# Optimization experiments

Measured on AMD Instinct MI355X. Metric: run time of the kernel, lower is better.

## Reference

```python
import jax, jax.numpy as jnp
import numpy as np

N_NODES = 50000
N_EDGES = 800000
IN_F = 512
H_F = 32
HEADS = 8
N_CLS = 40
NEG_SLOPE = 0.2


def gat_conv(h, W, al, ar, b, src, dst, n_heads, d_out):
    """DGL-style GATConv. h: [N, F_in]; W: [F_in, n_heads*d_out];
    al, ar: [n_heads, d_out]; b: [n_heads*d_out]. Returns [N, n_heads, d_out]."""
    n = h.shape[0]
    feat = (h @ W).reshape(n, n_heads, d_out)            # [N, H, D]
    el = jnp.sum(feat * al[None], axis=-1)               # [N, H]
    er = jnp.sum(feat * ar[None], axis=-1)               # [N, H]
    e = jax.nn.leaky_relu(el[src] + er[dst], NEG_SLOPE)  # [E, H]
    # numerically stable edge softmax per destination node
    m = jax.ops.segment_max(e, dst, num_segments=n)      # [N, H]
    m = jnp.where(jnp.isfinite(m), m, 0.0)
    ee = jnp.exp(e - m[dst])                             # [E, H]
    den = jax.ops.segment_sum(ee, dst, num_segments=n)   # [N, H]
    alpha = ee / jnp.maximum(den[dst], 1e-9)             # [E, H]
    msg = alpha[:, :, None] * feat[src]                  # [E, H, D]
    rst = jax.ops.segment_sum(msg, dst, num_segments=n)  # [N, H, D]
    return rst + b.reshape(1, n_heads, d_out)


def setup_inputs() -> dict:
    key = jax.random.key(0)
    ks = jax.random.split(key, 16)
    hid = H_F * HEADS
    s = lambda fan: 1.0 / np.sqrt(fan)
    return {
        "in_feat": jax.random.normal(ks[0], (N_NODES, IN_F), jnp.float32),
        "src": jax.random.randint(ks[1], (N_EDGES,), 0, N_NODES, jnp.int32),
        "dst": jax.random.randint(ks[2], (N_EDGES,), 0, N_NODES, jnp.int32),
        "W0": jax.random.normal(ks[3], (IN_F, hid), jnp.float32) * s(IN_F),
        "al0": jax.random.normal(ks[4], (HEADS, H_F), jnp.float32) * s(H_F),
        "ar0": jax.random.normal(ks[5], (HEADS, H_F), jnp.float32) * s(H_F),
        "b0": jnp.zeros((hid,), jnp.float32),
        "W1": jax.random.normal(ks[6], (hid, hid), jnp.float32) * s(hid),
        "al1": jax.random.normal(ks[7], (HEADS, H_F), jnp.float32) * s(H_F),
        "ar1": jax.random.normal(ks[8], (HEADS, H_F), jnp.float32) * s(H_F),
        "b1": jnp.zeros((hid,), jnp.float32),
        "W2": jax.random.normal(ks[9], (hid, N_CLS), jnp.float32) * s(hid),
        "al2": jax.random.normal(ks[10], (1, N_CLS), jnp.float32) * s(N_CLS),
        "ar2": jax.random.normal(ks[11], (1, N_CLS), jnp.float32) * s(N_CLS),
        "b2": jnp.zeros((N_CLS,), jnp.float32),
    }


def reference(in_feat, src, dst, W0, al0, ar0, b0, W1, al1, ar1, b1,
              W2, al2, ar2, b2):
    n = in_feat.shape[0]
    # layer 0 + ReLU (dropout p=0.0 is identity) + flatten heads
    h = gat_conv(in_feat, W0, al0, ar0, b0, src, dst, HEADS, H_F)
    h = jax.nn.relu(h).reshape(n, -1)
    # layer 1
    h = gat_conv(h, W1, al1, ar1, b1, src, dst, HEADS, H_F)
    h = jax.nn.relu(h).reshape(n, -1)
    # output layer, single head, no activation
    h = gat_conv(h, W2, al2, ar2, b2, src, dst, 1, N_CLS)
    return h.reshape(n, -1)
```

## Files before the change

kernel.cpp:

```cpp
#include <hip/hip_runtime.h>
#include <hip/hip_bf16.h>

#define N_NODES 50000
#define N_EDGES 800000
#define IN_F 512
#define HID 256
#define HEADS 8
#define DHEAD 32
#define N_CLS 40
#define NCLS_PAD 64

typedef __bf16 bf16x8 __attribute__((ext_vector_type(8)));
typedef float f32x4 __attribute__((ext_vector_type(4)));

#define AT_AL0 0
#define AT_AR0 256
#define AT_AL1 512
#define AT_AR1 768
#define AT_AL2 1024
#define AT_AR2 1088
#define AT_B0  1152
#define AT_B1  1408
#define AT_B2  1664
#define AT_SZ  1792

__device__ __forceinline__ float ldflag(const void* p, long long i, int isbf) {
  return isbf ? __bfloat162float(((const __hip_bfloat16*)p)[i])
              : ((const float*)p)[i];
}
__device__ __forceinline__ float blo(unsigned u) { return __uint_as_float(u << 16); }
__device__ __forceinline__ float bhi(unsigned u) { return __uint_as_float(u & 0xffff0000u); }
__device__ __forceinline__ unsigned pk2(float a, float b) {
  unsigned x = __bfloat16_as_ushort(__float2bfloat16(a));
  unsigned y = __bfloat16_as_ushort(__float2bfloat16(b));
  return x | (y << 16);
}

__global__ void k_detect_prep(const unsigned short* __restrict__ raw, int* __restrict__ flag,
                              const void* al0, const void* ar0, const void* al1, const void* ar1,
                              const void* al2, const void* ar2, const void* b0, const void* b1,
                              const void* b2, float* __restrict__ att, int* __restrict__ cursor) {
  __shared__ int cnt[256];
  int t = threadIdx.x;
  for (int i = t; i < N_NODES; i += 256) cursor[i] = 0;
  int c = 0;
  for (int i = t; i < 8192; i += 256) {
    int e = (raw[i] >> 7) & 0xFF;
    if (e >= 0x90) c++;
  }
  cnt[t] = c;
  __syncthreads();
  for (int s = 128; s; s >>= 1) {
    if (t < s) cnt[t] += cnt[t + s];
    __syncthreads();
  }
  __shared__ int sflag;
  if (t == 0) { sflag = (cnt[0] > 64) ? 0 : 1; *flag = sflag; }
  __syncthreads();
  int isbf = sflag;
  att[AT_AL0 + t] = ldflag(al0, t, isbf);
  att[AT_AR0 + t] = ldflag(ar0, t, isbf);
  att[AT_AL1 + t] = ldflag(al1, t, isbf);
  att[AT_AR1 + t] = ldflag(ar1, t, isbf);
  att[AT_B0 + t]  = ldflag(b0, t, isbf);
  att[AT_B1 + t]  = ldflag(b1, t, isbf);
  if (t < N_CLS) {
    att[AT_AL2 + t] = ldflag(al2, t, isbf);
    att[AT_AR2 + t] = ldflag(ar2, t, isbf);
    att[AT_B2 + t]  = ldflag(b2, t, isbf);
  }
}

__global__ void k_hist(const int* __restrict__ dst, int* __restrict__ cnt) {
  int e = blockIdx.x * blockDim.x + threadIdx.x;
  if (e < N_EDGES) atomicAdd(&cnt[dst[e]], 1);
}

#define SCAN_B 512
#define SCAN_NB ((N_NODES + SCAN_B - 1) / SCAN_B)

__global__ __launch_bounds__(SCAN_B) void k_scan_blocks(const int* __restrict__ deg,
                                                        int* __restrict__ excl,
                                                        int* __restrict__ partial) {
  __shared__ int buf[SCAN_B];
  int t = threadIdx.x;
  int i = blockIdx.x * SCAN_B + t;
  int v = (i < N_NODES) ? deg[i] : 0;
  buf[t] = v;
  __syncthreads();
  for (int off = 1; off < SCAN_B; off <<= 1) {
    int x = (t >= off) ? buf[t - off] : 0;
    __syncthreads();
    buf[t] += x;
    __syncthreads();
  }
  if (i < N_NODES) excl[i] = buf[t] - v;
  if (t == SCAN_B - 1) partial[blockIdx.x] = buf[t];
}

__global__ void k_scan_partials(int* __restrict__ partial, int* __restrict__ rowptr) {
  __shared__ int buf[SCAN_NB];
  int t = threadIdx.x;
  if (t < SCAN_NB) buf[t] = partial[t];
  __syncthreads();
  if (t == 0) {
    int run = 0;
    for (int b = 0; b < SCAN_NB; b++) { int v = buf[b]; buf[b] = run; run += v; }
    rowptr[N_NODES] = run;
  }
  __syncthreads();
  if (t < SCAN_NB) partial[t] = buf[t];
}

__global__ void k_scan_add(int* __restrict__ rowptr, const int* __restrict__ partial,
                           int* __restrict__ cursor) {
  int i = blockIdx.x * blockDim.x + threadIdx.x;
  if (i < N_NODES) {
    rowptr[i] += partial[i / SCAN_B];
    cursor[i] = 0;
  }
}

__global__ void k_scatter(const int* __restrict__ src, const int* __restrict__ dst,
                          const int* __restrict__ rowptr, int* __restrict__ cursor,
                          int* __restrict__ csr_src) {
  int e = blockIdx.x * blockDim.x + threadIdx.x;
  if (e < N_EDGES) {
    int d = dst[e];
    int pos = rowptr[d] + atomicAdd(&cursor[d], 1);
    csr_src[pos] = src[e];
  }
}

#define TW0 (HID * IN_F)
#define TW1 (TW0 + HID * HID)
#define TW2 (TW1 + NCLS_PAD * HID)
__global__ void k_transpose_all(const void* __restrict__ W0, const void* __restrict__ W1,
                                const void* __restrict__ W2,
                                __hip_bfloat16* __restrict__ w0t, __hip_bfloat16* __restrict__ w1t,
                                __hip_bfloat16* __restrict__ w2t, const int* __restrict__ flag) {
  int isbf = *flag;
  int i = blockIdx.x * blockDim.x + threadIdx.x;
  if (i < TW0) {
    int n = i >> 9, k = i & 511;
    w0t[i] = __float2bfloat16(ldflag(W0, (long long)k * HID + n, isbf));
  } else if (i < TW1) {
    int j = i - TW0;
    int n = j >> 8, k = j & 255;
    w1t[j] = __float2bfloat16(ldflag(W1, (long long)k * HID + n, isbf));
  } else if (i < TW2) {
    int j = i - TW1;
    int n = j >> 8, k = j & 255;
    float v = (n < N_CLS) ? ldflag(W2, (long long)k * N_CLS + n, isbf) : 0.f;
    w2t[j] = __float2bfloat16(v);
  }
}

__device__ __forceinline__ uint4 loadA(const void* A, int isbf, int ga, int M, int K, int off) {
  uint4 av = make_uint4(0u, 0u, 0u, 0u);
  if (ga < M) {
    if (isbf) {
      av = *(const uint4*)((const __hip_bfloat16*)A + (size_t)ga * K + off);
    } else {
      const float* ap = (const float*)A + (size_t)ga * K + off;
      float4 f1 = *(const float4*)ap;
      float4 f2 = *(const float4*)(ap + 4);
      av.x = pk2(f1.x, f1.y); av.y = pk2(f1.z, f1.w);
      av.z = pk2(f2.x, f2.y); av.w = pk2(f2.z, f2.w);
    }
  }
  return av;
}

__global__ __launch_bounds__(256) void k_gemm64(const void* __restrict__ A,
                                                const __hip_bfloat16* __restrict__ Bt,
                                                __hip_bfloat16* __restrict__ C,
                                                int M, int K, int N,
                                                const int* __restrict__ flag, int force_bf,
                                                const float* __restrict__ al,
                                                const float* __restrict__ ar,
                                                float* __restrict__ el,
                                                float* __restrict__ er, int fuse_eler) {
  __shared__ unsigned short As[64][40];
  __shared__ unsigned short Bs[64][40];
  const int isbf = force_bf ? 1 : *flag;
  int nblk = N >> 6;
  int per = nblk << 3;
  int g = blockIdx.x / per;
  int i2 = blockIdx.x - g * per;
  int mb = g * 8 + (i2 & 7);
  int nb = i2 >> 3;
  int m0 = mb * 64, n0 = nb * 64;
  if (m0 >= M) return;
  int tid = threadIdx.x;
  int lrow = tid >> 2;
  int lcol = (tid & 3) * 8;
  int wave = tid >> 6, lane = tid & 63;
  int wm = (wave >> 1) * 32, wn = (wave & 1) * 32;
  int lm = lane & 15, quad = lane >> 4;
  f32x4 acc[2][2] = {};
  uint4 av = loadA(A, isbf, m0 + lrow, M, K, lcol);
  uint4 bv = *(const uint4*)(Bt + (size_t)(n0 + lrow) * K + lcol);
  for (int k0 = 0; k0 < K; k0 += 32) {
    __syncthreads();
    *(uint4*)(&As[lrow][lcol]) = av;
    *(uint4*)(&Bs[lrow][lcol]) = bv;
    __syncthreads();
    uint4 avn = make_uint4(0u, 0u, 0u, 0u), bvn = make_uint4(0u, 0u, 0u, 0u);
    if (k0 + 32 < K) {
      avn = loadA(A, isbf, m0 + lrow, M, K, k0 + 32 + lcol);
      bvn = *(const uint4*)(Bt + (size_t)(n0 + lrow) * K + k0 + 32 + lcol);
    }
    bf16x8 af[2], bfr[2];
    #pragma unroll
    for (int i = 0; i < 2; i++) {
      af[i]  = *(const bf16x8*)(&As[wm + i * 16 + lm][quad * 8]);
      bfr[i] = *(const bf16x8*)(&Bs[wn + i * 16 + lm][quad * 8]);
    }
    #pragma unroll
    for (int mi = 0; mi < 2; mi++)
      #pragma unroll
      for (int ni = 0; ni < 2; ni++)
        acc[mi][ni] = __builtin_amdgcn_mfma_f32_16x16x32_bf16(af[mi], bfr[ni], acc[mi][ni], 0, 0, 0);
    av = avn; bv = bvn;
  }
  #pragma unroll
  for (int mi = 0; mi < 2; mi++)
    #pragma unroll
    for (int ni = 0; ni < 2; ni++)
      #pragma unroll
      for (int r = 0; r < 4; r++) {
        int gm = m0 + wm + mi * 16 + quad * 4 + r;
        int gn = n0 + wn + ni * 16 + lm;
        if (gm < M) C[(size_t)gm * N + gn] = __float2bfloat16(acc[mi][ni][r]);
      }
  if (fuse_eler) {
    int hg = (n0 + wn) >> 5;
    float ala[2], ara[2];
    #pragma unroll
    for (int ni = 0; ni < 2; ni++) {
      ala[ni] = al[hg * DHEAD + ni * 16 + lm];
      ara[ni] = ar[hg * DHEAD + ni * 16 + lm];
    }
    #pragma unroll
    for (int mi = 0; mi < 2; mi++)
      #pragma unroll
      for (int r = 0; r < 4; r++) {
        float pl = acc[mi][0][r] * ala[0] + acc[mi][1][r] * ala[1];
        float pr = acc[mi][0][r] * ara[0] + acc[mi][1][r] * ara[1];
        #pragma unroll
        for (int d = 1; d < 16; d <<= 1) {
          pl += __shfl_xor(pl, d, 16);
          pr += __shfl_xor(pr, d, 16);
        }
        int gm = m0 + wm + mi * 16 + quad * 4 + r;
        if (lm == 0 && gm < M) {
          el[gm * HEADS + hg] = pl;
          er[gm * HEADS + hg] = pr;
        }
      }
  }
}

__global__ void k_eler2(const __hip_bfloat16* __restrict__ feat2,
                        const float* __restrict__ al, const float* __restrict__ ar,
                        float* __restrict__ el, float* __restrict__ er) {
  int n = blockIdx.x * blockDim.x + threadIdx.x;
  if (n >= N_NODES) return;
  const __hip_bfloat16* f = feat2 + (size_t)n * NCLS_PAD;
  float sl = 0.f, sr = 0.f;
  for (int d = 0; d < N_CLS; d++) {
    float v = __bfloat162float(f[d]);
    sl += v * al[d];
    sr += v * ar[d];
  }
  el[n] = sl;
  er[n] = sr;
}

__global__ __launch_bounds__(256) void k_aggregate8(const int* __restrict__ rowptr,
                                                    const int* __restrict__ csr_src,
                                                    const uint4* __restrict__ feat_rows,
                                                    const float* __restrict__ el,
                                                    const float* __restrict__ er,
                                                    const float* __restrict__ bias,
                                                    __hip_bfloat16* __restrict__ out) {
  __shared__ float lds_acc[8][256];
  __shared__ float lds_l[8][32];
  int n = blockIdx.x;
  int t = threadIdx.x;
  int slot = t >> 5;
  int c = t & 31;
  int hh = c >> 2;
  float er_n = er[n * HEADS + hh];
  int beg = rowptr[n], end = rowptr[n + 1];
  float l = 0.f;
  float acc[8] = {0.f, 0.f, 0.f, 0.f, 0.f, 0.f, 0.f, 0.f};
  int i = beg + slot;
  for (; i + 8 < end; i += 16) {
    int s1 = csr_src[i];
    int s2 = csr_src[i + 8];
    float el1 = el[s1 * HEADS + hh];
    float el2 = el[s2 * HEADS + hh];
    uint4 f1 = feat_rows[(size_t)s1 * 32 + c];
    uint4 f2 = feat_rows[(size_t)s2 * 32 + c];
    float x1 = el1 + er_n, x2 = el2 + er_n;
    float e1 = x1 > 0.f ? x1 : 0.2f * x1;
    float e2 = x2 > 0.f ? x2 : 0.2f * x2;
    float p1 = __expf(fminf(e1, 60.f));
    float p2 = __expf(fminf(e2, 60.f));
    l += p1 + p2;
    acc[0] += p1 * blo(f1.x) + p2 * blo(f2.x); acc[1] += p1 * bhi(f1.x) + p2 * bhi(f2.x);
    acc[2] += p1 * blo(f1.y) + p2 * blo(f2.y); acc[3] += p1 * bhi(f1.y) + p2 * bhi(f2.y);
    acc[4] += p1 * blo(f1.z) + p2 * blo(f2.z); acc[5] += p1 * bhi(f1.z) + p2 * bhi(f2.z);
    acc[6] += p1 * blo(f1.w) + p2 * blo(f2.w); acc[7] += p1 * bhi(f1.w) + p2 * bhi(f2.w);
  }
  if (i < end) {
    int s = csr_src[i];
    float elv = el[s * HEADS + hh];
    uint4 fv = feat_rows[(size_t)s * 32 + c];
    float x = elv + er_n;
    float e = x > 0.f ? x : 0.2f * x;
    float p = __expf(fminf(e, 60.f));
    l += p;
    acc[0] += p * blo(fv.x); acc[1] += p * bhi(fv.x);
    acc[2] += p * blo(fv.y); acc[3] += p * bhi(fv.y);
    acc[4] += p * blo(fv.z); acc[5] += p * bhi(fv.z);
    acc[6] += p * blo(fv.w); acc[7] += p * bhi(fv.w);
  }
  *(float4*)&lds_acc[slot][c * 8]     = make_float4(acc[0], acc[1], acc[2], acc[3]);
  *(float4*)&lds_acc[slot][c * 8 + 4] = make_float4(acc[4], acc[5], acc[6], acc[7]);
  lds_l[slot][c] = l;
  __syncthreads();
  float a = 0.f, L = 0.f;
  #pragma unroll
  for (int s2 = 0; s2 < 8; s2++) { a += lds_acc[s2][t]; L += lds_l[s2][t >> 3]; }
  float o = a / fmaxf(L, 1e-9f) + bias[t];
  o = fmaxf(o, 0.f);
  out[(size_t)n * HID + t] = __float2bfloat16(o);
}

__global__ __launch_bounds__(256) void k_aggregate1(const int* __restrict__ rowptr,
                                                    const int* __restrict__ csr_src,
                                                    const uint4* __restrict__ fr2,
                                                    const float* __restrict__ el,
                                                    const float* __restrict__ er,
                                                    const float* __restrict__ bias,
                                                    void* __restrict__ out,
                                                    const int* __restrict__ flag) {
  __shared__ float lds_acc[32][64];
  __shared__ float lds_l[32][8];
  int isbf = *flag;
  int n = blockIdx.x;
  int t = threadIdx.x;
  int slot = t >> 3;
  int c = t & 7;
  float er_n = er[n];
  int beg = rowptr[n], end = rowptr[n + 1];
  float l = 0.f;
  float acc[8] = {0.f, 0.f, 0.f, 0.f, 0.f, 0.f, 0.f, 0.f};
  int i = beg + slot;
  for (; i + 32 < end; i += 64) {
    int s1 = csr_src[i], s2 = csr_src[i + 32];
    float el1 = el[s1], el2 = el[s2];
    uint4 f1 = fr2[(size_t)s1 * 8 + c];
    uint4 f2 = fr2[(size_t)s2 * 8 + c];
    float x1 = el1 + er_n, x2 = el2 + er_n;
    float e1 = x1 > 0.f ? x1 : 0.2f * x1;
    float e2 = x2 > 0.f ? x2 : 0.2f * x2;
    float p1 = __expf(fminf(e1, 60.f));
    float p2 = __expf(fminf(e2, 60.f));
    l += p1 + p2;
    acc[0] += p1 * blo(f1.x) + p2 * blo(f2.x); acc[1] += p1 * bhi(f1.x) + p2 * bhi(f2.x);
    acc[2] += p1 * blo(f1.y) + p2 * blo(f2.y); acc[3] += p1 * bhi(f1.y) + p2 * bhi(f2.y);
    acc[4] += p1 * blo(f1.z) + p2 * blo(f2.z); acc[5] += p1 * bhi(f1.z) + p2 * bhi(f2.z);
    acc[6] += p1 * blo(f1.w) + p2 * blo(f2.w); acc[7] += p1 * bhi(f1.w) + p2 * bhi(f2.w);
  }
  if (i < end) {
    int s = csr_src[i];
    float x = el[s] + er_n;
    uint4 fv = fr2[(size_t)s * 8 + c];
    float e = x > 0.f ? x : 0.2f * x;
    float p = __expf(fminf(e, 60.f));
    l += p;
    acc[0] += p * blo(fv.x); acc[1] += p * bhi(fv.x);
    acc[2] += p * blo(fv.y); acc[3] += p * bhi(fv.y);
    acc[4] += p * blo(fv.z); acc[5] += p * bhi(fv.z);
    acc[6] += p * blo(fv.w); acc[7] += p * bhi(fv.w);
  }
  *(float4*)&lds_acc[slot][c * 8]     = make_float4(acc[0], acc[1], acc[2], acc[3]);
  *(float4*)&lds_acc[slot][c * 8 + 4] = make_float4(acc[4], acc[5], acc[6], acc[7]);
  lds_l[slot][c] = l;
  __syncthreads();
  if (t < N_CLS) {
    float a = 0.f, L = 0.f;
    #pragma unroll
    for (int s2 = 0; s2 < 32; s2++) { a += lds_acc[s2][t]; L += lds_l[s2][t >> 3]; }
    float o = a / fmaxf(L, 1e-9f) + bias[t];
    if (isbf) ((__hip_bfloat16*)out)[(size_t)n * N_CLS + t] = __float2bfloat16(o);
    else      ((float*)out)[(size_t)n * N_CLS + t] = o;
  }
}

static inline size_t align_up(size_t x) { return (x + 255) & ~(size_t)255; }

extern "C" void kernel_launch(void* const* d_in, const int* in_sizes, int n_in,
                              void* d_out, int out_size, void* d_ws, size_t ws_size,
                              hipStream_t stream) {
  const void* in_feat = d_in[0];
  const int* src = (const int*)d_in[1];
  const int* dst = (const int*)d_in[2];
  const void* W0  = d_in[3];
  const void* al0 = d_in[4];
  const void* ar0 = d_in[5];
  const void* b0  = d_in[6];
  const void* W1  = d_in[7];
  const void* al1 = d_in[8];
  const void* ar1 = d_in[9];
  const void* b1  = d_in[10];
  const void* W2  = d_in[11];
  const void* al2 = d_in[12];
  const void* ar2 = d_in[13];
  const void* b2  = d_in[14];

  char* p = (char*)d_ws;
  int* flag = (int*)p;                   p += 256;
  float* att = (float*)p;                p += align_up(AT_SZ * sizeof(float));
  int* rowptr = (int*)p;                 p += align_up((N_NODES + 1) * sizeof(int));
  int* cursor = (int*)p;                 p += align_up(N_NODES * sizeof(int));
  int* csr_src = (int*)p;                p += align_up(N_EDGES * sizeof(int));
  int* partial = (int*)p;                p += align_up(SCAN_NB * sizeof(int));
  __hip_bfloat16* feat16 = (__hip_bfloat16*)p; p += align_up((size_t)N_NODES * HID * sizeof(__hip_bfloat16));
  __hip_bfloat16* h16 = (__hip_bfloat16*)p;    p += align_up((size_t)N_NODES * HID * sizeof(__hip_bfloat16));
  float* el = (float*)p;                 p += align_up((size_t)N_NODES * HEADS * sizeof(float));
  float* er = (float*)p;                 p += align_up((size_t)N_NODES * HEADS * sizeof(float));
  __hip_bfloat16* w0t = (__hip_bfloat16*)p;    p += align_up((size_t)HID * IN_F * sizeof(__hip_bfloat16));
  __hip_bfloat16* w1t = (__hip_bfloat16*)p;    p += align_up((size_t)HID * HID * sizeof(__hip_bfloat16));
  __hip_bfloat16* w2t = (__hip_bfloat16*)p;    p += align_up((size_t)NCLS_PAD * HID * sizeof(__hip_bfloat16));

  const int EB = (N_EDGES + 255) / 256;
  const int MB64 = (N_NODES + 63) / 64;
  const int GROUPS = (MB64 + 7) / 8;
  const int G4 = GROUPS * 8 * 4;
  const int G1 = GROUPS * 8 * 1;

  k_detect_prep<<<1, 256, 0, stream>>>((const unsigned short*)in_feat, flag,
                                       al0, ar0, al1, ar1, al2, ar2, b0, b1, b2, att, cursor);

  k_hist<<<EB, 256, 0, stream>>>(dst, cursor);
  k_scan_blocks<<<SCAN_NB, SCAN_B, 0, stream>>>(cursor, rowptr, partial);
  k_scan_partials<<<1, 128, 0, stream>>>(partial, rowptr);
  k_scan_add<<<(N_NODES + 255) / 256, 256, 0, stream>>>(rowptr, partial, cursor);
  k_scatter<<<EB, 256, 0, stream>>>(src, dst, rowptr, cursor, csr_src);

  k_transpose_all<<<(TW2 + 255) / 256, 256, 0, stream>>>(W0, W1, W2, w0t, w1t, w2t, flag);

  k_gemm64<<<G4, 256, 0, stream>>>(in_feat, w0t, feat16, N_NODES, IN_F, HID, flag, 0,
                                   att + AT_AL0, att + AT_AR0, el, er, 1);
  k_aggregate8<<<N_NODES, 256, 0, stream>>>(rowptr, csr_src, (const uint4*)feat16, el, er, att + AT_B0, h16);

  k_gemm64<<<G4, 256, 0, stream>>>(h16, w1t, feat16, N_NODES, HID, HID, flag, 1,
                                   att + AT_AL1, att + AT_AR1, el, er, 1);
  k_aggregate8<<<N_NODES, 256, 0, stream>>>(rowptr, csr_src, (const uint4*)feat16, el, er, att + AT_B1, h16);

  k_gemm64<<<G1, 256, 0, stream>>>(h16, w2t, feat16, N_NODES, HID, NCLS_PAD, flag, 1,
                                   nullptr, nullptr, nullptr, nullptr, 0);
  k_eler2<<<(N_NODES + 255) / 256, 256, 0, stream>>>(feat16, att + AT_AL2, att + AT_AR2, el, er);
  k_aggregate1<<<N_NODES, 256, 0, stream>>>(rowptr, csr_src, (const uint4*)feat16, el, er, att + AT_B2, d_out, flag);
}
```

Baseline: 531.9 us.

## Add 128x128 MFMA GEMM with direct-to-LDS loads and packed aggregation math

Adds a new 128x128-tile bf16 MFMA GEMM that uses global_load_lds for direct global-to-LDS copies, XCD-aware block remapping, and a fused el/er reduction, and uses it for the first two layers in place of the 64-tile kernel. It also changes the aggregation kernels to use packed float2 accumulation and 32-bit shift-based address arithmetic. The aim is more data reuse per tile, fewer address and FMA instructions, and better L2 locality. The trade-offs are a larger tile with fewer blocks in flight, a single-buffered LDS loop, and 32-bit offsets that rely on the node count staying small.

Measured after the change: 554.5 us. 1.04x slower.

```diff
diff --git a/kernel.cpp b/kernel.cpp
--- a/kernel.cpp
+++ b/kernel.cpp
@@ -12,6 +12,7 @@
 
 typedef __bf16 bf16x8 __attribute__((ext_vector_type(8)));
 typedef float f32x4 __attribute__((ext_vector_type(4)));
+typedef float f32x2 __attribute__((ext_vector_type(2)));
 
 #define AT_AL0 0
 #define AT_AR0 256
@@ -30,10 +31,20 @@
 }
 __device__ __forceinline__ float blo(unsigned u) { return __uint_as_float(u << 16); }
 __device__ __forceinline__ float bhi(unsigned u) { return __uint_as_float(u & 0xffff0000u); }
+__device__ __forceinline__ f32x2 bpair(unsigned u) {
+  f32x2 r;
+  r.x = __uint_as_float(u << 16);
+  r.y = __uint_as_float(u & 0xffff0000u);
+  return r;
+}
 __device__ __forceinline__ unsigned pk2(float a, float b) {
   unsigned x = __bfloat16_as_ushort(__float2bfloat16(a));
   unsigned y = __bfloat16_as_ushort(__float2bfloat16(b));
   return x | (y << 16);
+}
+__device__ __forceinline__ void gload16(const unsigned short* g, unsigned short* l) {
+  __builtin_amdgcn_global_load_lds((__attribute__((address_space(1))) void*)g,
+                                   (__attribute__((address_space(3))) void*)l, 16, 0, 0);
 }
 
 __global__ void k_detect_prep(const unsigned short* __restrict__ raw, int* __restrict__ flag,
@@ -170,6 +181,130 @@
     }
   }
   return av;
+}
+
+__global__ __launch_bounds__(256) void k_gemm128(const void* __restrict__ A,
+                                                 const __hip_bfloat16* __restrict__ Bt,
+                                                 __hip_bfloat16* __restrict__ C,
+                                                 int M, int K, int N,
+                                                 const int* __restrict__ flag, int force_bf,
+                                                 const float* __restrict__ al,
+                                                 const float* __restrict__ ar,
+                                                 float* __restrict__ el,
+                                                 float* __restrict__ er, int fuse_eler) {
+  __shared__ unsigned short sA[128 * 32];
+  __shared__ unsigned short sB[128 * 32];
+  const int isbf = force_bf ? 1 : *flag;
+  int nwg = gridDim.x;
+  int q = nwg >> 3, r = nwg & 7;
+  int xcd = blockIdx.x & 7, lid = blockIdx.x >> 3;
+  int logical = (xcd < r ? xcd * (q + 1) : r * (q + 1) + (xcd - r) * q) + lid;
+  int nblk = N >> 7;
+  int mb = logical / nblk;
+  int nb = logical - mb * nblk;
+  int m0 = mb * 128, n0 = nb * 128;
+  int tid = threadIdx.x;
+  int wave = tid >> 6, lane = tid & 63;
+  int wm = (wave >> 1) * 64, wn = (wave & 1) * 64;
+  int lm = lane & 15, quad = lane >> 4;
+  int c0 = (wave << 7) + lane, c1 = c0 + 64;
+  int rA0 = c0 >> 2, rA1 = c1 >> 2;
+  int col0 = (c0 & 3) << 3, col1 = (c1 & 3) << 3;
+  int gr0 = m0 + rA0; if (gr0 > M - 1) gr0 = M - 1;
+  int gr1 = m0 + rA1; if (gr1 > M - 1) gr1 = M - 1;
+  const unsigned short* Ab = (const unsigned short*)A;
+  const float* Af = (const float*)A;
+  const unsigned short* Bb = (const unsigned short*)Bt;
+  size_t aog0 = (size_t)gr0 * K + col0;
+  size_t aog1 = (size_t)gr1 * K + col1;
+  size_t bog0 = (size_t)(n0 + rA0) * K + col0;
+  size_t bog1 = (size_t)(n0 + rA1) * K + col1;
+  unsigned short* la0 = &sA[c0 << 3];
+  unsigned short* la1 = &sA[c1 << 3];
+  unsigned short* lb0 = &sB[c0 << 3];
+  unsigned short* lb1 = &sB[c1 << 3];
+  const char* sAb = (const char*)sA;
+  const char* sBb = (const char*)sB;
+  int fq = quad << 4;
+  int aoff[4], boff[4];
+  #pragma unroll
+  for (int i = 0; i < 4; i++) {
+    aoff[i] = ((wm + i * 16 + lm) << 6) + fq;
+    boff[i] = ((wn + i * 16 + lm) << 6) + fq;
+  }
+  f32x4 acc[4][4] = {};
+  for (int k0 = 0; k0 < K; k0 += 32) {
+    __syncthreads();
+    if (isbf) {
+      gload16(Ab + aog0 + k0, la0);
+      gload16(Ab + aog1 + k0, la1);
+    } else {
+      const float* p0 = Af + aog0 + k0;
+      const float* p1 = Af + aog1 + k0;
+      float4 x0 = *(const float4*)p0, y0 = *(const float4*)(p0 + 4);
+      float4 x1 = *(const float4*)p1, y1 = *(const float4*)(p1 + 4);
+      *(uint4*)la0 = make_uint4(pk2(x0.x, x0.y), pk2(x0.z, x0.w), pk2(y0.x, y0.y), pk2(y0.z, y0.w));
+      *(uint4*)la1 = make_uint4(pk2(x1.x, x1.y), pk2(x1.z, x1.w), pk2(y1.x, y1.y), pk2(y1.z, y1.w));
+    }
+    gload16(Bb + bog0 + k0, lb0);
+    gload16(Bb + bog1 + k0, lb1);
+    __syncthreads();
+    bf16x8 af[4], bfr[4];
+    #pragma unroll
+    for (int i = 0; i < 4; i++) {
+      af[i]  = *(const bf16x8*)(sAb + aoff[i]);
+      bfr[i] = *(const bf16x8*)(sBb + boff[i]);
+    }
+    #pragma unroll
+    for (int mi = 0; mi < 4; mi++)
+      #pragma unroll
+      for (int ni = 0; ni < 4; ni++)
+        acc[mi][ni] = __builtin_amdgcn_mfma_f32_16x16x32_bf16(af[mi], bfr[ni], acc[mi][ni], 0, 0, 0);
+  }
+  #pragma unroll
+  for (int mi = 0; mi < 4; mi++) {
+    #pragma unroll
+    for (int r2 = 0; r2 < 4; r2++) {
+      int gm = m0 + wm + mi * 16 + (quad << 2) + r2;
+      if (gm < M) {
+        #pragma unroll
+        for (int ni = 0; ni < 4; ni++) {
+          int gn = n0 + wn + ni * 16 + lm;
+          C[(size_t)gm * N + gn] = __float2bfloat16(acc[mi][ni][r2]);
+        }
+      }
+    }
+  }
+  if (fuse_eler) {
+    int h0 = (n0 + wn) >> 5;
+    float ala[4], ara[4];
+    #pragma unroll
+    for (int ni = 0; ni < 4; ni++) {
+      int idx = (h0 + (ni >> 1)) * DHEAD + ((ni & 1) << 4) + lm;
+      ala[ni] = al[idx];
+      ara[ni] = ar[idx];
+    }
+    #pragma unroll
+    for (int mi = 0; mi < 4; mi++)
+      #pragma unroll
+      for (int r2 = 0; r2 < 4; r2++) {
+        int gm = m0 + wm + mi * 16 + (quad << 2) + r2;
+        #pragma unroll
+        for (int hp = 0; hp < 2; hp++) {
+          float pl = acc[mi][2 * hp][r2] * ala[2 * hp] + acc[mi][2 * hp + 1][r2] * ala[2 * hp + 1];
+          float pr = acc[mi][2 * hp][r2] * ara[2 * hp] + acc[mi][2 * hp + 1][r2] * ara[2 * hp + 1];
+          #pragma unroll
+          for (int d = 1; d < 16; d <<= 1) {
+            pl += __shfl_xor(pl, d, 16);
+            pr += __shfl_xor(pr, d, 16);
+          }
+          if (lm == 0 && gm < M) {
+            el[gm * HEADS + h0 + hp] = pl;
+            er[gm * HEADS + h0 + hp] = pr;
+          }
+        }
+      }
+  }
 }
 
 __global__ __launch_bounds__(256) void k_gemm64(const void* __restrict__ A,
@@ -295,41 +430,41 @@
   float er_n = er[n * HEADS + hh];
   int beg = rowptr[n], end = rowptr[n + 1];
   float l = 0.f;
-  float acc[8] = {0.f, 0.f, 0.f, 0.f, 0.f, 0.f, 0.f, 0.f};
+  f32x2 a0 = {0.f, 0.f}, a1 = {0.f, 0.f}, a2 = {0.f, 0.f}, a3 = {0.f, 0.f};
+  const char* fb = (const char*)feat_rows;
+  unsigned cb = (unsigned)c << 4;
   int i = beg + slot;
   for (; i + 8 < end; i += 16) {
     int s1 = csr_src[i];
     int s2 = csr_src[i + 8];
     float el1 = el[s1 * HEADS + hh];
     float el2 = el[s2 * HEADS + hh];
-    uint4 f1 = feat_rows[(size_t)s1 * 32 + c];
-    uint4 f2 = feat_rows[(size_t)s2 * 32 + c];
+    uint4 f1 = *(const uint4*)(fb + (((unsigned)s1 << 9) | cb));
+    uint4 f2 = *(const uint4*)(fb + (((unsigned)s2 << 9) | cb));
     float x1 = el1 + er_n, x2 = el2 + er_n;
     float e1 = x1 > 0.f ? x1 : 0.2f * x1;
     float e2 = x2 > 0.f ? x2 : 0.2f * x2;
     float p1 = __expf(fminf(e1, 60.f));
     float p2 = __expf(fminf(e2, 60.f));
     l += p1 + p2;
-    acc[0] += p1 * blo(f1.x) + p2 * blo(f2.x); acc[1] += p1 * bhi(f1.x) + p2 * bhi(f2.x);
-    acc[2] += p1 * blo(f1.y) + p2 * blo(f2.y); acc[3] += p1 * bhi(f1.y) + p2 * bhi(f2.y);
-    acc[4] += p1 * blo(f1.z) + p2 * blo(f2.z); acc[5] += p1 * bhi(f1.z) + p2 * bhi(f2.z);
-    acc[6] += p1 * blo(f1.w) + p2 * blo(f2.w); acc[7] += p1 * bhi(f1.w) + p2 * bhi(f2.w);
+    a0 += bpair(f1.x) * p1; a1 += bpair(f1.y) * p1;
+    a2 += bpair(f1.z) * p1; a3 += bpair(f1.w) * p1;
+    a0 += bpair(f2.x) * p2; a1 += bpair(f2.y) * p2;
+    a2 += bpair(f2.z) * p2; a3 += bpair(f2.w) * p2;
   }
   if (i < end) {
     int s = csr_src[i];
     float elv = el[s * HEADS + hh];
-    uint4 fv = feat_rows[(size_t)s * 32 + c];
+    uint4 fv = *(const uint4*)(fb + (((unsigned)s << 9) | cb));
     float x = elv + er_n;
     float e = x > 0.f ? x : 0.2f * x;
     float p = __expf(fminf(e, 60.f));
     l += p;
-    acc[0] += p * blo(fv.x); acc[1] += p * bhi(fv.x);
-    acc[2] += p * blo(fv.y); acc[3] += p * bhi(fv.y);
-    acc[4] += p * blo(fv.z); acc[5] += p * bhi(fv.z);
-    acc[6] += p * blo(fv.w); acc[7] += p * bhi(fv.w);
-  }
-  *(float4*)&lds_acc[slot][c * 8]     = make_float4(acc[0], acc[1], acc[2], acc[3]);
-  *(float4*)&lds_acc[slot][c * 8 + 4] = make_float4(acc[4], acc[5], acc[6], acc[7]);
+    a0 += bpair(fv.x) * p; a1 += bpair(fv.y) * p;
+    a2 += bpair(fv.z) * p; a3 += bpair(fv.w) * p;
+  }
+  *(float4*)&lds_acc[slot][c * 8]     = make_float4(a0.x, a0.y, a1.x, a1.y);
+  *(float4*)&lds_acc[slot][c * 8 + 4] = make_float4(a2.x, a2.y, a3.x, a3.y);
   lds_l[slot][c] = l;
   __syncthreads();
   float a = 0.f, L = 0.f;
@@ -358,38 +493,38 @@
   float er_n = er[n];
   int beg = rowptr[n], end = rowptr[n + 1];
   float l = 0.f;
-  float acc[8] = {0.f, 0.f, 0.f, 0.f, 0.f, 0.f, 0.f, 0.f};
+  f32x2 a0 = {0.f, 0.f}, a1 = {0.f, 0.f}, a2 = {0.f, 0.f}, a3 = {0.f, 0.f};
+  const char* fb = (const char*)fr2;
+  unsigned cb = (unsigned)c << 4;
   int i = beg + slot;
   for (; i + 32 < end; i += 64) {
     int s1 = csr_src[i], s2 = csr_src[i + 32];
     float el1 = el[s1], el2 = el[s2];
-    uint4 f1 = fr2[(size_t)s1 * 8 + c];
-    uint4 f2 = fr2[(size_t)s2 * 8 + c];
+    uint4 f1 = *(const uint4*)(fb + (((unsigned)s1 << 7) | cb));
+    uint4 f2 = *(const uint4*)(fb + (((unsigned)s2 << 7) | cb));
     float x1 = el1 + er_n, x2 = el2 + er_n;
     float e1 = x1 > 0.f ? x1 : 0.2f * x1;
     float e2 = x2 > 0.f ? x2 : 0.2f * x2;
     float p1 = __expf(fminf(e1, 60.f));
     float p2 = __expf(fminf(e2, 60.f));
     l += p1 + p2;
-    acc[0] += p1 * blo(f1.x) + p2 * blo(f2.x); acc[1] += p1 * bhi(f1.x) + p2 * bhi(f2.x);
-    acc[2] += p1 * blo(f1.y) + p2 * blo(f2.y); acc[3] += p1 * bhi(f1.y) + p2 * bhi(f2.y);
-    acc[4] += p1 * blo(f1.z) + p2 * blo(f2.z); acc[5] += p1 * bhi(f1.z) + p2 * bhi(f2.z);
-    acc[6] += p1 * blo(f1.w) + p2 * blo(f2.w); acc[7] += p1 * bhi(f1.w) + p2 * bhi(f2.w);
+    a0 += bpair(f1.x) * p1; a1 += bpair(f1.y) * p1;
+    a2 += bpair(f1.z) * p1; a3 += bpair(f1.w) * p1;
+    a0 += bpair(f2.x) * p2; a1 += bpair(f2.y) * p2;
+    a2 += bpair(f2.z) * p2; a3 += bpair(f2.w) * p2;
   }
   if (i < end) {
     int s = csr_src[i];
     float x = el[s] + er_n;
-    uint4 fv = fr2[(size_t)s * 8 + c];
+    uint4 fv = *(const uint4*)(fb + (((unsigned)s << 7) | cb));
     float e = x > 0.f ? x : 0.2f * x;
     float p = __expf(fminf(e, 60.f));
     l += p;
-    acc[0] += p * blo(fv.x); acc[1] += p * bhi(fv.x);
-    acc[2] += p * blo(fv.y); acc[3] += p * bhi(fv.y);
-    acc[4] += p * blo(fv.z); acc[5] += p * bhi(fv.z);
-    acc[6] += p * blo(fv.w); acc[7] += p * bhi(fv.w);
-  }
-  *(float4*)&lds_acc[slot][c * 8]     = make_float4(acc[0], acc[1], acc[2], acc[3]);
-  *(float4*)&lds_acc[slot][c * 8 + 4] = make_float4(acc[4], acc[5], acc[6], acc[7]);
+    a0 += bpair(fv.x) * p; a1 += bpair(fv.y) * p;
+    a2 += bpair(fv.z) * p; a3 += bpair(fv.w) * p;
+  }
+  *(float4*)&lds_acc[slot][c * 8]     = make_float4(a0.x, a0.y, a1.x, a1.y);
+  *(float4*)&lds_acc[slot][c * 8 + 4] = make_float4(a2.x, a2.y, a3.x, a3.y);
   lds_l[slot][c] = l;
   __syncthreads();
   if (t < N_CLS) {
@@ -441,8 +576,9 @@
   const int EB = (N_EDGES + 255) / 256;
   const int MB64 = (N_NODES + 63) / 64;
   const int GROUPS = (MB64 + 7) / 8;
-  const int G4 = GROUPS * 8 * 4;
   const int G1 = GROUPS * 8 * 1;
+  const int MB128 = (N_NODES + 127) / 128;
+  const int GX = MB128 * 2;
 
   k_detect_prep<<<1, 256, 0, stream>>>((const unsigned short*)in_feat, flag,
                                        al0, ar0, al1, ar1, al2, ar2, b0, b1, b2, att, cursor);
@@ -455,12 +591,12 @@
 
   k_transpose_all<<<(TW2 + 255) / 256, 256, 0, stream>>>(W0, W1, W2, w0t, w1t, w2t, flag);
 
-  k_gemm64<<<G4, 256, 0, stream>>>(in_feat, w0t, feat16, N_NODES, IN_F, HID, flag, 0,
-                                   att + AT_AL0, att + AT_AR0, el, er, 1);
+  k_gemm128<<<GX, 256, 0, stream>>>(in_feat, w0t, feat16, N_NODES, IN_F, HID, flag, 0,
+                                    att + AT_AL0, att + AT_AR0, el, er, 1);
   k_aggregate8<<<N_NODES, 256, 0, stream>>>(rowptr, csr_src, (const uint4*)feat16, el, er, att + AT_B0, h16);
 
-  k_gemm64<<<G4, 256, 0, stream>>>(h16, w1t, feat16, N_NODES, HID, HID, flag, 1,
-                                   att + AT_AL1, att + AT_AR1, el, er, 1);
+  k_gemm128<<<GX, 256, 0, stream>>>(h16, w1t, feat16, N_NODES, HID, HID, flag, 1,
+                                    att + AT_AL1, att + AT_AR1, el, er, 1);
   k_aggregate8<<<N_NODES, 256, 0, stream>>>(rowptr, csr_src, (const uint4*)feat16, el, er, att + AT_B1, h16);
 
   k_gemm64<<<G1, 256, 0, stream>>>(h16, w2t, feat16, N_NODES, HID, NCLS_PAD, flag, 1,
```

## Replace LDS-tiled GEMM with per-wave 64x64 register-direct MFMA GEMM

Applied to the files above, without the earlier changes.

The shared-memory tiled GEMM, where each block computed a 64x64 tile with four waves of 32x32, is replaced. In the new kernel each wave computes a full 64x64 output tile on its own, loading A and B fragments straight from global memory into registers with one-step prefetch. This removes the LDS staging and the two block barriers per k-step, but each wave now issues more redundant global loads and holds more accumulator registers. The aggregation kernels also switch to packed float2 accumulation and shift/or address arithmetic for gathering feature rows.

Measured after the change: 625.4 us. 1.18x slower.

```diff
diff --git a/kernel.cpp b/kernel.cpp
--- a/kernel.cpp
+++ b/kernel.cpp
@@ -12,6 +12,7 @@
 
 typedef __bf16 bf16x8 __attribute__((ext_vector_type(8)));
 typedef float f32x4 __attribute__((ext_vector_type(4)));
+typedef float f32x2 __attribute__((ext_vector_type(2)));
 
 #define AT_AL0 0
 #define AT_AR0 256
@@ -30,10 +31,26 @@
 }
 __device__ __forceinline__ float blo(unsigned u) { return __uint_as_float(u << 16); }
 __device__ __forceinline__ float bhi(unsigned u) { return __uint_as_float(u & 0xffff0000u); }
+__device__ __forceinline__ f32x2 bpair(unsigned u) {
+  f32x2 r;
+  r.x = __uint_as_float(u << 16);
+  r.y = __uint_as_float(u & 0xffff0000u);
+  return r;
+}
 __device__ __forceinline__ unsigned pk2(float a, float b) {
   unsigned x = __bfloat16_as_ushort(__float2bfloat16(a));
   unsigned y = __bfloat16_as_ushort(__float2bfloat16(b));
   return x | (y << 16);
+}
+__device__ __forceinline__ uint4 ldA8(const void* A, int isbf, size_t base) {
+  if (isbf) return *(const uint4*)((const unsigned short*)A + base);
+  const float* ap = (const float*)A + base;
+  float4 f1 = *(const float4*)ap;
+  float4 f2 = *(const float4*)(ap + 4);
+  return make_uint4(pk2(f1.x, f1.y), pk2(f1.z, f1.w), pk2(f2.x, f2.y), pk2(f2.z, f2.w));
+}
+__device__ __forceinline__ bf16x8 as_bf(uint4 v) {
+  union { uint4 u; bf16x8 b; } x; x.u = v; return x.b;
 }
 
 __global__ void k_detect_prep(const unsigned short* __restrict__ raw, int* __restrict__ flag,
@@ -156,107 +173,103 @@
   }
 }
 
-__device__ __forceinline__ uint4 loadA(const void* A, int isbf, int ga, int M, int K, int off) {
-  uint4 av = make_uint4(0u, 0u, 0u, 0u);
-  if (ga < M) {
-    if (isbf) {
-      av = *(const uint4*)((const __hip_bfloat16*)A + (size_t)ga * K + off);
-    } else {
-      const float* ap = (const float*)A + (size_t)ga * K + off;
-      float4 f1 = *(const float4*)ap;
-      float4 f2 = *(const float4*)(ap + 4);
-      av.x = pk2(f1.x, f1.y); av.y = pk2(f1.z, f1.w);
-      av.z = pk2(f2.x, f2.y); av.w = pk2(f2.z, f2.w);
-    }
-  }
-  return av;
-}
-
-__global__ __launch_bounds__(256) void k_gemm64(const void* __restrict__ A,
-                                                const __hip_bfloat16* __restrict__ Bt,
-                                                __hip_bfloat16* __restrict__ C,
-                                                int M, int K, int N,
-                                                const int* __restrict__ flag, int force_bf,
-                                                const float* __restrict__ al,
-                                                const float* __restrict__ ar,
-                                                float* __restrict__ el,
-                                                float* __restrict__ er, int fuse_eler) {
-  __shared__ unsigned short As[64][40];
-  __shared__ unsigned short Bs[64][40];
+__global__ __launch_bounds__(256) void k_gemmw(const void* __restrict__ A,
+                                               const __hip_bfloat16* __restrict__ Bt,
+                                               __hip_bfloat16* __restrict__ C,
+                                               int M, int K, int N,
+                                               const int* __restrict__ flag, int force_bf,
+                                               const float* __restrict__ al,
+                                               const float* __restrict__ ar,
+                                               float* __restrict__ el,
+                                               float* __restrict__ er, int fuse_eler) {
   const int isbf = force_bf ? 1 : *flag;
   int nblk = N >> 6;
-  int per = nblk << 3;
-  int g = blockIdx.x / per;
-  int i2 = blockIdx.x - g * per;
-  int mb = g * 8 + (i2 & 7);
-  int nb = i2 >> 3;
+  int wave = threadIdx.x >> 6, lane = threadIdx.x & 63;
+  int tile = blockIdx.x * 4 + wave;
+  int mb = tile / nblk;
+  int nb = tile - mb * nblk;
   int m0 = mb * 64, n0 = nb * 64;
   if (m0 >= M) return;
-  int tid = threadIdx.x;
-  int lrow = tid >> 2;
-  int lcol = (tid & 3) * 8;
-  int wave = tid >> 6, lane = tid & 63;
-  int wm = (wave >> 1) * 32, wn = (wave & 1) * 32;
   int lm = lane & 15, quad = lane >> 4;
-  f32x4 acc[2][2] = {};
-  uint4 av = loadA(A, isbf, m0 + lrow, M, K, lcol);
-  uint4 bv = *(const uint4*)(Bt + (size_t)(n0 + lrow) * K + lcol);
-  for (int k0 = 0; k0 < K; k0 += 32) {
-    __syncthreads();
-    *(uint4*)(&As[lrow][lcol]) = av;
-    *(uint4*)(&Bs[lrow][lcol]) = bv;
-    __syncthreads();
-    uint4 avn = make_uint4(0u, 0u, 0u, 0u), bvn = make_uint4(0u, 0u, 0u, 0u);
-    if (k0 + 32 < K) {
-      avn = loadA(A, isbf, m0 + lrow, M, K, k0 + 32 + lcol);
-      bvn = *(const uint4*)(Bt + (size_t)(n0 + lrow) * K + k0 + 32 + lcol);
+  int koff = quad << 3;
+  size_t ab[4];
+  const unsigned short* bb[4];
+  #pragma unroll
+  for (int i = 0; i < 4; i++) {
+    int ga = m0 + i * 16 + lm;
+    if (ga > M - 1) ga = M - 1;
+    ab[i] = (size_t)ga * K + koff;
+    bb[i] = (const unsigned short*)Bt + (size_t)(n0 + i * 16 + lm) * K + koff;
+  }
+  f32x4 acc[4][4] = {};
+  uint4 a0[4], b0[4];
+  #pragma unroll
+  for (int i = 0; i < 4; i++) { a0[i] = ldA8(A, isbf, ab[i]); b0[i] = *(const uint4*)bb[i]; }
+  int nk = K >> 5;
+  for (int t = 1; t < nk; ++t) {
+    int k0 = t << 5;
+    uint4 a1[4], b1[4];
+    #pragma unroll
+    for (int i = 0; i < 4; i++) {
+      a1[i] = ldA8(A, isbf, ab[i] + k0);
+      b1[i] = *(const uint4*)(bb[i] + k0);
     }
-    bf16x8 af[2], bfr[2];
-    #pragma unroll
-    for (int i = 0; i < 2; i++) {
-      af[i]  = *(const bf16x8*)(&As[wm + i * 16 + lm][quad * 8]);
-      bfr[i] = *(const bf16x8*)(&Bs[wn + i * 16 + lm][quad * 8]);
+    #pragma unroll
+    for (int mi = 0; mi < 4; mi++)
+      #pragma unroll
+      for (int ni = 0; ni < 4; ni++)
+        acc[mi][ni] = __builtin_amdgcn_mfma_f32_16x16x32_bf16(as_bf(a0[mi]), as_bf(b0[ni]),
+                                                              acc[mi][ni], 0, 0, 0);
+    #pragma unroll
+    for (int i = 0; i < 4; i++) { a0[i] = a1[i]; b0[i] = b1[i]; }
+  }
+  #pragma unroll
+  for (int mi = 0; mi < 4; mi++)
+    #pragma unroll
+    for (int ni = 0; ni < 4; ni++)
+      acc[mi][ni] = __builtin_amdgcn_mfma_f32_16x16x32_bf16(as_bf(a0[mi]), as_bf(b0[ni]),
+                                                            acc[mi][ni], 0, 0, 0);
+  #pragma unroll
+  for (int mi = 0; mi < 4; mi++) {
+    #pragma unroll
+    for (int r2 = 0; r2 < 4; r2++) {
+      int gm = m0 + mi * 16 + (quad << 2) + r2;
+      if (gm < M) {
+        #pragma unroll
+        for (int ni = 0; ni < 4; ni++) {
+          int gn = n0 + ni * 16 + lm;
+          C[(size_t)gm * N + gn] = __float2bfloat16(acc[mi][ni][r2]);
+        }
+      }
     }
-    #pragma unroll
-    for (int mi = 0; mi < 2; mi++)
+  }
+  if (fuse_eler) {
+    int h0 = n0 >> 5;
+    float ala[4], ara[4];
+    #pragma unroll
+    for (int ni = 0; ni < 4; ni++) {
+      int idx = (h0 + (ni >> 1)) * DHEAD + ((ni & 1) << 4) + lm;
+      ala[ni] = al[idx];
+      ara[ni] = ar[idx];
+    }
+    #pragma unroll
+    for (int mi = 0; mi < 4; mi++)
       #pragma unroll
-      for (int ni = 0; ni < 2; ni++)
-        acc[mi][ni] = __builtin_amdgcn_mfma_f32_16x16x32_bf16(af[mi], bfr[ni], acc[mi][ni], 0, 0, 0);
-    av = avn; bv = bvn;
-  }
-  #pragma unroll
-  for (int mi = 0; mi < 2; mi++)
-    #pragma unroll
-    for (int ni = 0; ni < 2; ni++)
-      #pragma unroll
-      for (int r = 0; r < 4; r++) {
-        int gm = m0 + wm + mi * 16 + quad * 4 + r;
-        int gn = n0 + wn + ni * 16 + lm;
-        if (gm < M) C[(size_t)gm * N + gn] = __float2bfloat16(acc[mi][ni][r]);
-      }
-  if (fuse_eler) {
-    int hg = (n0 + wn) >> 5;
-    float ala[2], ara[2];
-    #pragma unroll
-    for (int ni = 0; ni < 2; ni++) {
-      ala[ni] = al[hg * DHEAD + ni * 16 + lm];
-      ara[ni] = ar[hg * DHEAD + ni * 16 + lm];
-    }
-    #pragma unroll
-    for (int mi = 0; mi < 2; mi++)
-      #pragma unroll
-      for (int r = 0; r < 4; r++) {
-        float pl = acc[mi][0][r] * ala[0] + acc[mi][1][r] * ala[1];
-        float pr = acc[mi][0][r] * ara[0] + acc[mi][1][r] * ara[1];
+      for (int r2 = 0; r2 < 4; r2++) {
+        int gm = m0 + mi * 16 + (quad << 2) + r2;
         #pragma unroll
-        for (int d = 1; d < 16; d <<= 1) {
-          pl += __shfl_xor(pl, d, 16);
-          pr += __shfl_xor(pr, d, 16);
-        }
-        int gm = m0 + wm + mi * 16 + quad * 4 + r;
-        if (lm == 0 && gm < M) {
-          el[gm * HEADS + hg] = pl;
-          er[gm * HEADS + hg] = pr;
+        for (int hp = 0; hp < 2; hp++) {
+          float pl = acc[mi][2 * hp][r2] * ala[2 * hp] + acc[mi][2 * hp + 1][r2] * ala[2 * hp + 1];
+          float pr = acc[mi][2 * hp][r2] * ara[2 * hp] + acc[mi][2 * hp + 1][r2] * ara[2 * hp + 1];
+          #pragma unroll
+          for (int d = 1; d < 16; d <<= 1) {
+            pl += __shfl_xor(pl, d, 16);
+            pr += __shfl_xor(pr, d, 16);
+          }
+          if (lm == 0 && gm < M) {
+            el[gm * HEADS + h0 + hp] = pl;
+            er[gm * HEADS + h0 + hp] = pr;
+          }
         }
       }
   }
@@ -295,41 +308,41 @@
   float er_n = er[n * HEADS + hh];
   int beg = rowptr[n], end = rowptr[n + 1];
   float l = 0.f;
-  float acc[8] = {0.f, 0.f, 0.f, 0.f, 0.f, 0.f, 0.f, 0.f};
+  f32x2 a0 = {0.f, 0.f}, a1 = {0.f, 0.f}, a2 = {0.f, 0.f}, a3 = {0.f, 0.f};
+  const char* fb = (const char*)feat_rows;
+  unsigned cb = (unsigned)c << 4;
   int i = beg + slot;
   for (; i + 8 < end; i += 16) {
     int s1 = csr_src[i];
     int s2 = csr_src[i + 8];
     float el1 = el[s1 * HEADS + hh];
     float el2 = el[s2 * HEADS + hh];
-    uint4 f1 = feat_rows[(size_t)s1 * 32 + c];
-    uint4 f2 = feat_rows[(size_t)s2 * 32 + c];
+    uint4 f1 = *(const uint4*)(fb + (((unsigned)s1 << 9) | cb));
+    uint4 f2 = *(const uint4*)(fb + (((unsigned)s2 << 9) | cb));
     float x1 = el1 + er_n, x2 = el2 + er_n;
     float e1 = x1 > 0.f ? x1 : 0.2f * x1;
     float e2 = x2 > 0.f ? x2 : 0.2f * x2;
     float p1 = __expf(fminf(e1, 60.f));
     float p2 = __expf(fminf(e2, 60.f));
     l += p1 + p2;
-    acc[0] += p1 * blo(f1.x) + p2 * blo(f2.x); acc[1] += p1 * bhi(f1.x) + p2 * bhi(f2.x);
-    acc[2] += p1 * blo(f1.y) + p2 * blo(f2.y); acc[3] += p1 * bhi(f1.y) + p2 * bhi(f2.y);
-    acc[4] += p1 * blo(f1.z) + p2 * blo(f2.z); acc[5] += p1 * bhi(f1.z) + p2 * bhi(f2.z);
-    acc[6] += p1 * blo(f1.w) + p2 * blo(f2.w); acc[7] += p1 * bhi(f1.w) + p2 * bhi(f2.w);
+    a0 += bpair(f1.x) * p1; a1 += bpair(f1.y) * p1;
+    a2 += bpair(f1.z) * p1; a3 += bpair(f1.w) * p1;
+    a0 += bpair(f2.x) * p2; a1 += bpair(f2.y) * p2;
+    a2 += bpair(f2.z) * p2; a3 += bpair(f2.w) * p2;
   }
   if (i < end) {
     int s = csr_src[i];
     float elv = el[s * HEADS + hh];
-    uint4 fv = feat_rows[(size_t)s * 32 + c];
+    uint4 fv = *(const uint4*)(fb + (((unsigned)s << 9) | cb));
     float x = elv + er_n;
     float e = x > 0.f ? x : 0.2f * x;
     float p = __expf(fminf(e, 60.f));
     l += p;
-    acc[0] += p * blo(fv.x); acc[1] += p * bhi(fv.x);
-    acc[2] += p * blo(fv.y); acc[3] += p * bhi(fv.y);
-    acc[4] += p * blo(fv.z); acc[5] += p * bhi(fv.z);
-    acc[6] += p * blo(fv.w); acc[7] += p * bhi(fv.w);
-  }
-  *(float4*)&lds_acc[slot][c * 8]     = make_float4(acc[0], acc[1], acc[2], acc[3]);
-  *(float4*)&lds_acc[slot][c * 8 + 4] = make_float4(acc[4], acc[5], acc[6], acc[7]);
+    a0 += bpair(fv.x) * p; a1 += bpair(fv.y) * p;
+    a2 += bpair(fv.z) * p; a3 += bpair(fv.w) * p;
+  }
+  *(float4*)&lds_acc[slot][c * 8]     = make_float4(a0.x, a0.y, a1.x, a1.y);
+  *(float4*)&lds_acc[slot][c * 8 + 4] = make_float4(a2.x, a2.y, a3.x, a3.y);
   lds_l[slot][c] = l;
   __syncthreads();
   float a = 0.f, L = 0.f;
@@ -358,38 +371,38 @@
   float er_n = er[n];
   int beg = rowptr[n], end = rowptr[n + 1];
   float l = 0.f;
-  float acc[8] = {0.f, 0.f, 0.f, 0.f, 0.f, 0.f, 0.f, 0.f};
+  f32x2 a0 = {0.f, 0.f}, a1 = {0.f, 0.f}, a2 = {0.f, 0.f}, a3 = {0.f, 0.f};
+  const char* fb = (const char*)fr2;
+  unsigned cb = (unsigned)c << 4;
   int i = beg + slot;
   for (; i + 32 < end; i += 64) {
     int s1 = csr_src[i], s2 = csr_src[i + 32];
     float el1 = el[s1], el2 = el[s2];
-    uint4 f1 = fr2[(size_t)s1 * 8 + c];
-    uint4 f2 = fr2[(size_t)s2 * 8 + c];
+    uint4 f1 = *(const uint4*)(fb + (((unsigned)s1 << 7) | cb));
+    uint4 f2 = *(const uint4*)(fb + (((unsigned)s2 << 7) | cb));
     float x1 = el1 + er_n, x2 = el2 + er_n;
     float e1 = x1 > 0.f ? x1 : 0.2f * x1;
     float e2 = x2 > 0.f ? x2 : 0.2f * x2;
     float p1 = __expf(fminf(e1, 60.f));
     float p2 = __expf(fminf(e2, 60.f));
     l += p1 + p2;
-    acc[0] += p1 * blo(f1.x) + p2 * blo(f2.x); acc[1] += p1 * bhi(f1.x) + p2 * bhi(f2.x);
-    acc[2] += p1 * blo(f1.y) + p2 * blo(f2.y); acc[3] += p1 * bhi(f1.y) + p2 * bhi(f2.y);
-    acc[4] += p1 * blo(f1.z) + p2 * blo(f2.z); acc[5] += p1 * bhi(f1.z) + p2 * bhi(f2.z);
-    acc[6] += p1 * blo(f1.w) + p2 * blo(f2.w); acc[7] += p1 * bhi(f1.w) + p2 * bhi(f2.w);
+    a0 += bpair(f1.x) * p1; a1 += bpair(f1.y) * p1;
+    a2 += bpair(f1.z) * p1; a3 += bpair(f1.w) * p1;
+    a0 += bpair(f2.x) * p2; a1 += bpair(f2.y) * p2;
+    a2 += bpair(f2.z) * p2; a3 += bpair(f2.w) * p2;
   }
   if (i < end) {
     int s = csr_src[i];
     float x = el[s] + er_n;
-    uint4 fv = fr2[(size_t)s * 8 + c];
+    uint4 fv = *(const uint4*)(fb + (((unsigned)s << 7) | cb));
     float e = x > 0.f ? x : 0.2f * x;
     float p = __expf(fminf(e, 60.f));
     l += p;
-    acc[0] += p * blo(fv.x); acc[1] += p * bhi(fv.x);
-    acc[2] += p * blo(fv.y); acc[3] += p * bhi(fv.y);
-    acc[4] += p * blo(fv.z); acc[5] += p * bhi(fv.z);
-    acc[6] += p * blo(fv.w); acc[7] += p * bhi(fv.w);
-  }
-  *(float4*)&lds_acc[slot][c * 8]     = make_float4(acc[0], acc[1], acc[2], acc[3]);
-  *(float4*)&lds_acc[slot][c * 8 + 4] = make_float4(acc[4], acc[5], acc[6], acc[7]);
+    a0 += bpair(fv.x) * p; a1 += bpair(fv.y) * p;
+    a2 += bpair(fv.z) * p; a3 += bpair(fv.w) * p;
+  }
+  *(float4*)&lds_acc[slot][c * 8]     = make_float4(a0.x, a0.y, a1.x, a1.y);
+  *(float4*)&lds_acc[slot][c * 8 + 4] = make_float4(a2.x, a2.y, a3.x, a3.y);
   lds_l[slot][c] = l;
   __syncthreads();
   if (t < N_CLS) {
@@ -440,9 +453,8 @@
 
   const int EB = (N_EDGES + 255) / 256;
   const int MB64 = (N_NODES + 63) / 64;
-  const int GROUPS = (MB64 + 7) / 8;
-  const int G4 = GROUPS * 8 * 4;
-  const int G1 = GROUPS * 8 * 1;
+  const int GW01 = MB64;
+  const int GW2 = (MB64 + 3) / 4;
 
   k_detect_prep<<<1, 256, 0, stream>>>((const unsigned short*)in_feat, flag,
                                        al0, ar0, al1, ar1, al2, ar2, b0, b1, b2, att, cursor);
@@ -455,15 +467,15 @@
 
   k_transpose_all<<<(TW2 + 255) / 256, 256, 0, stream>>>(W0, W1, W2, w0t, w1t, w2t, flag);
 
-  k_gemm64<<<G4, 256, 0, stream>>>(in_feat, w0t, feat16, N_NODES, IN_F, HID, flag, 0,
-                                   att + AT_AL0, att + AT_AR0, el, er, 1);
+  k_gemmw<<<GW01, 256, 0, stream>>>(in_feat, w0t, feat16, N_NODES, IN_F, HID, flag, 0,
+                                    att + AT_AL0, att + AT_AR0, el, er, 1);
   k_aggregate8<<<N_NODES, 256, 0, stream>>>(rowptr, csr_src, (const uint4*)feat16, el, er, att + AT_B0, h16);
 
-  k_gemm64<<<G4, 256, 0, stream>>>(h16, w1t, feat16, N_NODES, HID, HID, flag, 1,
-                                   att + AT_AL1, att + AT_AR1, el, er, 1);
+  k_gemmw<<<GW01, 256, 0, stream>>>(h16, w1t, feat16, N_NODES, HID, HID, flag, 1,
+                                    att + AT_AL1, att + AT_AR1, el, er, 1);
   k_aggregate8<<<N_NODES, 256, 0, stream>>>(rowptr, csr_src, (const uint4*)feat16, el, er, att + AT_B1, h16);
 
-  k_gemm64<<<G1, 256, 0, stream>>>(h16, w2t, feat16, N_NODES, HID, NCLS_PAD, flag, 1,
+  k_gemmw<<<GW2, 256, 0, stream>>>(h16, w2t, feat16, N_NODES, HID, NCLS_PAD, flag, 1,
                                    nullptr, nullptr, nullptr, nullptr, 0);
   k_eler2<<<(N_NODES + 255) / 256, 256, 0, stream>>>(feat16, att + AT_AL2, att + AT_AR2, el, er);
   k_aggregate1<<<N_NODES, 256, 0, stream>>>(rowptr, csr_src, (const uint4*)feat16, el, er, att + AT_B2, d_out, flag);
```
